# Kernel optimization log

Hardware: AMD Instinct MI355X
Metric: run time of the kernel (lower is better)

## Reference

```python
import jax, jax.numpy as jnp
import numpy as np

# dims: heads, batch, seq (== maxSentenceSize), embed, key/query dim, value dim
H, B, S, E, DK, DV = 16, 4, 1024, 1024, 64, 64
SCALE = int(np.sqrt(DK))  # original uses int(np.sqrt(keySize)) == 8


def setup_inputs() -> dict:
    key = jax.random.key(0)
    k = jax.random.split(key, 5)
    embeddings = jax.random.normal(k[0], (B, S, E), jnp.float32)
    # original init: uniform(0, 1) weights
    Wq = jax.random.uniform(k[1], (H, E, DK), jnp.float32)
    Wk = jax.random.uniform(k[2], (H, E, DK), jnp.float32)
    # note: original valueWeights are also sized (E, keySize)
    Wv = jax.random.uniform(k[3], (H, E, DK), jnp.float32)
    Wo = jax.random.uniform(k[4], (H * DV, E), jnp.float32)
    return {"embeddings": embeddings, "Wq": Wq, "Wk": Wk, "Wv": Wv, "Wo": Wo}


def _causal_mask(s):
    # 0 on/below diagonal, -inf above (matches the torch list-comprehension mask)
    return jnp.where(jnp.tril(jnp.ones((s, s), bool)), 0.0, -jnp.inf).astype(jnp.float32)


def reference(embeddings, Wq, Wk, Wv, Wo):
    # per-head projections, all heads batched: [H,B,S,d]
    q = jnp.einsum('bse,hed->hbsd', embeddings, Wq)
    kk = jnp.einsum('bse,hed->hbsd', embeddings, Wk)
    v = jnp.einsum('bse,hed->hbsd', embeddings, Wv)
    # FAITHFUL to original: keys are RESHAPED (flat reinterpretation [S,DK]->[DK,S]
    # per (head,batch) slice), NOT transposed.
    kT = kk.reshape(H, B, DK, S)
    mask = _causal_mask(S)  # [S,S]
    # softmax((QK_reshaped + mask) / int(sqrt(keySize)))
    scores = (jnp.einsum('hbsd,hbdt->hbst', q, kT) + mask) / SCALE
    attn = jax.nn.softmax(scores, axis=-1)  # [H,B,S,S]
    av = jnp.einsum('hbst,hbtd->hbsd', attn, v)  # [H,B,S,DV]
    # FAITHFUL to original: flat reshape [H,B,S,DV] -> [B,S,DV*H]
    concat = av.reshape(B, S, DV * H)
    return concat @ Wo  # [B,S,E]
```

## Files before the change

kernel.cpp:

```cpp
#include <hip/hip_runtime.h>
#include <math.h>

#define H 16
#define B 4
#define S 1024
#define E 1024
#define DK 64

typedef _Float16 f16x8 __attribute__((ext_vector_type(8)));
typedef _Float16 f16x4 __attribute__((ext_vector_type(4)));
typedef float    f32x4 __attribute__((ext_vector_type(4)));

__device__ __forceinline__ int swzb(int row, int colByte) {
    return row * 128 + (colByte ^ ((row & 7) << 4));
}
__device__ __forceinline__ int swz32(int row, int colByte) {
    int slot = ((row & 3) ^ ((row >> 2) & 3)) << 4;
    return row * 64 + (colByte ^ slot);
}

__device__ __forceinline__ void split8(const float* __restrict__ p,
                                       f16x8& hi, f16x8& lo) {
    float4 a = *(const float4*)p;
    float4 b = *(const float4*)(p + 4);
    float x[8] = {a.x, a.y, a.z, a.w, b.x, b.y, b.z, b.w};
    #pragma unroll
    for (int j = 0; j < 8; ++j) {
        _Float16 h = (_Float16)x[j];
        hi[j] = h;
        lo[j] = (_Float16)(x[j] - (float)h);
    }
}

__global__ __launch_bounds__(256) void cvt_w(const float* __restrict__ Wq,
                                             const float* __restrict__ Wk,
                                             const float* __restrict__ Wv,
                                             _Float16* __restrict__ WTh,
                                             _Float16* __restrict__ WTl) {
    int et = blockIdx.x, chunk = blockIdx.y;
    const float* W = (chunk < 16 ? Wq : chunk < 32 ? Wk : Wv)
                     + (size_t)(chunk & 15) * E * DK;
    __shared__ _Float16 Th[64 * 64];
    __shared__ _Float16 Tl[64 * 64];
    int tid = threadIdx.x;
    #pragma unroll
    for (int rr = 0; rr < 4; ++rr) {
        int u = rr * 256 + tid;
        int ei = u >> 4, f4 = u & 15;
        float4 v = *(const float4*)&W[(size_t)(et * 64 + ei) * 64 + f4 * 4];
        float x[4] = {v.x, v.y, v.z, v.w};
        f16x4 h, l;
        #pragma unroll
        for (int j = 0; j < 4; ++j) {
            _Float16 hh = (_Float16)x[j];
            h[j] = hh;
            l[j] = (_Float16)(x[j] - (float)hh);
        }
        *(f16x4*)((char*)Th + swzb(ei, f4 * 8)) = h;
        *(f16x4*)((char*)Tl + swzb(ei, f4 * 8)) = l;
    }
    __syncthreads();
    #pragma unroll
    for (int rr = 0; rr < 2; ++rr) {
        int u = rr * 256 + tid;
        int d = u >> 3, e8 = u & 7;
        f16x8 oh, ol;
        #pragma unroll
        for (int j = 0; j < 8; ++j) {
            int ei = e8 * 8 + j;
            oh[j] = *(_Float16*)((char*)Th + swzb(ei, d * 2));
            ol[j] = *(_Float16*)((char*)Tl + swzb(ei, d * 2));
        }
        size_t idx = (size_t)(chunk * 64 + d) * 1024 + et * 64 + e8 * 8;
        *(f16x8*)&WTh[idx] = oh;
        if (chunk < 32) *(f16x8*)&WTl[idx] = ol;
    }
}

__global__ __launch_bounds__(256) void cvt_wo(const float* __restrict__ Wo,
                                              _Float16* __restrict__ WoT) {
    int kt = blockIdx.x, nt = blockIdx.y;
    __shared__ _Float16 T[64 * 64];
    int tid = threadIdx.x;
    #pragma unroll
    for (int rr = 0; rr < 4; ++rr) {
        int u = rr * 256 + tid;
        int ki = u >> 4, f4 = u & 15;
        float4 v = *(const float4*)&Wo[(size_t)(kt * 64 + ki) * 1024 + nt * 64 + f4 * 4];
        f16x4 o = { (_Float16)v.x, (_Float16)v.y, (_Float16)v.z, (_Float16)v.w };
        *(f16x4*)((char*)T + swzb(ki, f4 * 8)) = o;
    }
    __syncthreads();
    #pragma unroll
    for (int rr = 0; rr < 2; ++rr) {
        int u = rr * 256 + tid;
        int nl = u >> 3, k8 = u & 7;
        f16x8 o;
        #pragma unroll
        for (int j = 0; j < 8; ++j) {
            int ki = k8 * 8 + j;
            o[j] = *(_Float16*)((char*)T + swzb(ki, nl * 2));
        }
        *(f16x8*)&WoT[(size_t)(nt * 64 + nl) * 1024 + kt * 64 + k8 * 8] = o;
    }
}

__global__ __launch_bounds__(256) void gemm_qkv(
    const float* __restrict__ A, const _Float16* __restrict__ BTh,
    const _Float16* __restrict__ BTl,
    _Float16* __restrict__ QbH, _Float16* __restrict__ QbL,
    _Float16* __restrict__ kkTH, _Float16* __restrict__ kkTL,
    _Float16* __restrict__ V2) {
    __shared__ _Float16 AsH[128 * 32], AsL[128 * 32];
    __shared__ _Float16 BsH[128 * 32], BsL[128 * 32];
    const int NT = 24, cpx = 96;
    int wg = ((int)blockIdx.x & 7) * cpx + ((int)blockIdx.x >> 3);
    int mt = wg / NT, nt = wg % NT;
    const bool qk = (nt < 16);
    int r0 = mt * 128, c0 = nt * 128;
    int tid = threadIdx.x, lane = tid & 63, w = tid >> 6;
    int wr = w >> 1, wc = w & 1;
    int l15 = lane & 15, l4 = lane >> 4;

    f16x8 raH[2], raL[2], rbH[2], rbL[2];
    f32x4 zero = {0.f, 0.f, 0.f, 0.f};
    f32x4 acc[4][4];
    #pragma unroll
    for (int i = 0; i < 4; ++i)
        #pragma unroll
        for (int j = 0; j < 4; ++j) acc[i][j] = zero;

    #pragma unroll
    for (int rr = 0; rr < 2; ++rr) {
        int u = rr * 256 + tid, row = u >> 2, c8 = u & 3;
        split8(&A[(size_t)(r0 + row) * 1024 + c8 * 8], raH[rr], raL[rr]);
        rbH[rr] = *(const f16x8*)&BTh[(size_t)(c0 + row) * 1024 + c8 * 8];
        if (qk) rbL[rr] = *(const f16x8*)&BTl[(size_t)(c0 + row) * 1024 + c8 * 8];
    }

    for (int kt = 0; kt < 32; ++kt) {
        __syncthreads();
        #pragma unroll
        for (int rr = 0; rr < 2; ++rr) {
            int u = rr * 256 + tid, row = u >> 2, cb = (u & 3) * 16;
            int off = swz32(row, cb);
            *(f16x8*)((char*)AsH + off) = raH[rr];
            *(f16x8*)((char*)AsL + off) = raL[rr];
            *(f16x8*)((char*)BsH + off) = rbH[rr];
            if (qk) *(f16x8*)((char*)BsL + off) = rbL[rr];
        }
        if (kt < 31) {
            int k0 = (kt + 1) * 32;
            #pragma unroll
            for (int rr = 0; rr < 2; ++rr) {
                int u = rr * 256 + tid, row = u >> 2, c8 = u & 3;
                split8(&A[(size_t)(r0 + row) * 1024 + k0 + c8 * 8], raH[rr], raL[rr]);
                rbH[rr] = *(const f16x8*)&BTh[(size_t)(c0 + row) * 1024 + k0 + c8 * 8];
                if (qk) rbL[rr] = *(const f16x8*)&BTl[(size_t)(c0 + row) * 1024 + k0 + c8 * 8];
            }
        }
        __syncthreads();
        int kb = l4 * 16;
        f16x8 afH[4], afL[4], bfH[4], bfL[4];
        #pragma unroll
        for (int f = 0; f < 4; ++f) {
            int arow = wr * 64 + f * 16 + l15;
            int brow = wc * 64 + f * 16 + l15;
            afH[f] = *(const f16x8*)((char*)AsH + swz32(arow, kb));
            bfH[f] = *(const f16x8*)((char*)BsH + swz32(brow, kb));
            if (qk) {
                afL[f] = *(const f16x8*)((char*)AsL + swz32(arow, kb));
                bfL[f] = *(const f16x8*)((char*)BsL + swz32(brow, kb));
            }
        }
        #pragma unroll
        for (int i = 0; i < 4; ++i)
            #pragma unroll
            for (int j = 0; j < 4; ++j) {
                acc[i][j] = __builtin_amdgcn_mfma_f32_16x16x32_f16(
                    afH[i], bfH[j], acc[i][j], 0, 0, 0);
                if (qk) {
                    acc[i][j] = __builtin_amdgcn_mfma_f32_16x16x32_f16(
                        afH[i], bfL[j], acc[i][j], 0, 0, 0);
                    acc[i][j] = __builtin_amdgcn_mfma_f32_16x16x32_f16(
                        afL[i], bfH[j], acc[i][j], 0, 0, 0);
                }
            }
    }

    #pragma unroll
    for (int i = 0; i < 4; ++i) {
        int grow0 = r0 + wr * 64 + i * 16 + l4 * 4;
        #pragma unroll
        for (int j = 0; j < 4; ++j) {
            int gcol = c0 + wc * 64 + j * 16 + l15;
            if (gcol < 1024) {
                int hh = gcol >> 6, dk = gcol & 63;
                #pragma unroll
                for (int r = 0; r < 4; ++r) {
                    int grow = grow0 + r;
                    int bb = grow >> 10, s = grow & 1023;
                    float v = acc[i][j][r];
                    _Float16 h = (_Float16)v;
                    size_t idx = (((size_t)hh * 4 + bb) * 1024 + s) * 64 + dk;
                    QbH[idx] = h;
                    QbL[idx] = (_Float16)(v - (float)h);
                }
            } else if (gcol < 2048) {
                int hh = (gcol >> 6) & 15, dk = gcol & 63;
                #pragma unroll
                for (int r = 0; r < 4; ++r) {
                    int grow = grow0 + r;
                    int bb = grow >> 10, s = grow & 1023;
                    float v = acc[i][j][r];
                    _Float16 h = (_Float16)v;
                    size_t idx = (((size_t)hh * 4 + bb) * 64 + (s >> 4)) * 1024
                                 + (s & 15) * 64 + dk;
                    kkTH[idx] = h;
                    kkTL[idx] = (_Float16)(v - (float)h);
                }
            } else {
                int hh = (gcol >> 6) & 15, dv = gcol & 63;
                int bb = grow0 >> 10, s = grow0 & 1023;
                f16x4 o = { (_Float16)acc[i][j][0], (_Float16)acc[i][j][1],
                            (_Float16)acc[i][j][2], (_Float16)acc[i][j][3] };
                *(f16x4*)&V2[(((size_t)hh * 4 + bb) * 64 + dv) * 1024 + s] = o;
            }
        }
    }
}

__global__ __launch_bounds__(256) void trans_k(const _Float16* __restrict__ kkTH,
                                               const _Float16* __restrict__ kkTL,
                                               _Float16* __restrict__ K2H,
                                               _Float16* __restrict__ K2L) {
    int tt = blockIdx.x;
    size_t hb = blockIdx.y;
    int mode = blockIdx.z;
    const _Float16* src = mode ? kkTL : kkTH;
    _Float16* dst = mode ? K2L : K2H;
    __shared__ _Float16 T[64 * 64];
    int tid = threadIdx.x;
    #pragma unroll
    for (int rr = 0; rr < 2; ++rr) {
        int u = rr * 256 + tid;
        int d = u >> 3, c8 = u & 7;
        f16x8 v = *(const f16x8*)&src[(hb * 64 + d) * 1024 + tt * 64 + c8 * 8];
        *(f16x8*)((char*)T + swzb(d, c8 * 16)) = v;
    }
    __syncthreads();
    #pragma unroll
    for (int rr = 0; rr < 2; ++rr) {
        int u = rr * 256 + tid;
        int ti = u >> 3, d8 = u & 7;
        f16x8 o;
        #pragma unroll
        for (int j = 0; j < 8; ++j)
            o[j] = *(_Float16*)((char*)T + swzb(d8 * 8 + j, ti * 2));
        *(f16x8*)&dst[(hb * 1024 + tt * 64 + ti) * 64 + d8 * 8] = o;
    }
}

__global__ __launch_bounds__(256) void attn(
    const _Float16* __restrict__ QbH, const _Float16* __restrict__ QbL,
    const _Float16* __restrict__ K2H, const _Float16* __restrict__ K2L,
    const _Float16* __restrict__ V2, _Float16* __restrict__ CC) {
    int qt = blockIdx.x, b = blockIdx.y, h = blockIdx.z;
    size_t hb = (size_t)h * 4 + b;
    __shared__ _Float16 QsH[64 * 64], QsL[64 * 64];
    __shared__ _Float16 KsH[64 * 64], KsL[64 * 64];
    __shared__ _Float16 Vs[64 * 64], Ps[64 * 64];
    int tid = threadIdx.x, lane = tid & 63, w = tid >> 6;
    int l15 = lane & 15, l4 = lane >> 4;
    int s0 = qt * 64;

    #pragma unroll
    for (int rr = 0; rr < 2; ++rr) {
        int u = rr * 256 + tid, row = u >> 3, c8 = u & 7;
        size_t gi = (hb * 1024 + s0 + row) * 64 + c8 * 8;
        int off = swzb(row, c8 * 16);
        *(f16x8*)((char*)QsH + off) = *(const f16x8*)&QbH[gi];
        *(f16x8*)((char*)QsL + off) = *(const f16x8*)&QbL[gi];
    }
    __syncthreads();
    int srow = w * 16 + l15;
    f16x8 qfH[2], qfL[2];
    #pragma unroll
    for (int ks = 0; ks < 2; ++ks) {
        int kb = (ks * 32 + l4 * 8) * 2;
        qfH[ks] = *(const f16x8*)((char*)QsH + swzb(srow, kb));
        qfL[ks] = *(const f16x8*)((char*)QsL + swzb(srow, kb));
    }

    float m = -__builtin_inff(), lsum = 0.f;
    f32x4 zero = {0.f, 0.f, 0.f, 0.f};
    f32x4 acc2[4] = {zero, zero, zero, zero};
    int sg = s0 + srow;
    int ntile = qt + 1;

    for (int tt = 0; tt < ntile; ++tt) {
        int t0 = tt * 64;
        __syncthreads();
        #pragma unroll
        for (int rr = 0; rr < 2; ++rr) {
            int u = rr * 256 + tid, row = u >> 3, c8 = u & 7;
            int off = swzb(row, c8 * 16);
            size_t ki = (hb * 1024 + t0 + row) * 64 + c8 * 8;
            *(f16x8*)((char*)KsH + off) = *(const f16x8*)&K2H[ki];
            *(f16x8*)((char*)KsL + off) = *(const f16x8*)&K2L[ki];
            *(f16x8*)((char*)Vs + off) =
                *(const f16x8*)&V2[(hb * 64 + row) * 1024 + t0 + c8 * 8];
        }
        __syncthreads();

        f32x4 z[4] = {zero, zero, zero, zero};
        #pragma unroll
        for (int ks = 0; ks < 2; ++ks) {
            int kb = (ks * 32 + l4 * 8) * 2;
            #pragma unroll
            for (int f = 0; f < 4; ++f) {
                int trow = f * 16 + l15;
                f16x8 akH = *(const f16x8*)((char*)KsH + swzb(trow, kb));
                f16x8 akL = *(const f16x8*)((char*)KsL + swzb(trow, kb));
                z[f] = __builtin_amdgcn_mfma_f32_16x16x32_f16(akH, qfH[ks], z[f], 0, 0, 0);
                z[f] = __builtin_amdgcn_mfma_f32_16x16x32_f16(akH, qfL[ks], z[f], 0, 0, 0);
                z[f] = __builtin_amdgcn_mfma_f32_16x16x32_f16(akL, qfH[ks], z[f], 0, 0, 0);
            }
        }
        float mt = -__builtin_inff();
        #pragma unroll
        for (int f = 0; f < 4; ++f)
            #pragma unroll
            for (int r = 0; r < 4; ++r) {
                int tg = t0 + f * 16 + l4 * 4 + r;
                float val = z[f][r] * 0.125f;
                val = (tg > sg) ? -__builtin_inff() : val;
                z[f][r] = val;
                mt = fmaxf(mt, val);
            }
        mt = fmaxf(mt, __shfl_xor(mt, 16));
        mt = fmaxf(mt, __shfl_xor(mt, 32));
        float mn = fmaxf(m, mt);
        float corr = __expf(m - mn);
        float ps = 0.f;
        #pragma unroll
        for (int f = 0; f < 4; ++f)
            #pragma unroll
            for (int r = 0; r < 4; ++r) {
                float p = __expf(z[f][r] - mn);
                z[f][r] = p;
                ps += p;
            }
        ps += __shfl_xor(ps, 16);
        ps += __shfl_xor(ps, 32);
        lsum = lsum * corr + ps;
        m = mn;
        #pragma unroll
        for (int f = 0; f < 4; ++f) acc2[f] *= corr;

        #pragma unroll
        for (int f = 0; f < 4; ++f) {
            f16x4 pk = { (_Float16)z[f][0], (_Float16)z[f][1],
                         (_Float16)z[f][2], (_Float16)z[f][3] };
            *(f16x4*)((char*)Ps + swzb(srow, (f * 16 + l4 * 4) * 2)) = pk;
        }
        #pragma unroll
        for (int ks = 0; ks < 2; ++ks) {
            int kb = (ks * 32 + l4 * 8) * 2;
            f16x8 bp = *(const f16x8*)((char*)Ps + swzb(srow, kb));
            #pragma unroll
            for (int f = 0; f < 4; ++f) {
                int dvrow = f * 16 + l15;
                f16x8 av = *(const f16x8*)((char*)Vs + swzb(dvrow, kb));
                acc2[f] = __builtin_amdgcn_mfma_f32_16x16x32_f16(av, bp, acc2[f], 0, 0, 0);
            }
        }
    }

    float inv = 1.f / lsum;
    int sp = s0 + srow;
    int bprow = h >> 2;
    int spp = (h & 3) * 256 + b * 64 + (sp >> 4);
    int cb = (sp & 15) * 64;
    #pragma unroll
    for (int f = 0; f < 4; ++f) {
        int dv = f * 16 + l4 * 4;
        f16x4 o = { (_Float16)(acc2[f][0] * inv), (_Float16)(acc2[f][1] * inv),
                    (_Float16)(acc2[f][2] * inv), (_Float16)(acc2[f][3] * inv) };
        *(f16x4*)&CC[((size_t)bprow * 1024 + spp) * 1024 + cb + dv] = o;
    }
}

__global__ __launch_bounds__(256) void gemm_out(
    const _Float16* __restrict__ A, const _Float16* __restrict__ BT,
    float* __restrict__ out) {
    __shared__ _Float16 As[128 * 64];
    __shared__ _Float16 Bs[128 * 64];
    const int NT = 8, cpx = 32;
    int wg = ((int)blockIdx.x & 7) * cpx + ((int)blockIdx.x >> 3);
    int mt = wg / NT, nt = wg % NT;
    int r0 = mt * 128, c0 = nt * 128;
    int tid = threadIdx.x, lane = tid & 63, w = tid >> 6;
    int wr = w >> 1, wc = w & 1;
    int l15 = lane & 15, l4 = lane >> 4;

    f16x8 ra[4], rb[4];
    f32x4 zero = {0.f, 0.f, 0.f, 0.f};
    f32x4 acc[4][4];
    #pragma unroll
    for (int i = 0; i < 4; ++i)
        #pragma unroll
        for (int j = 0; j < 4; ++j) acc[i][j] = zero;

    #pragma unroll
    for (int rr = 0; rr < 4; ++rr) {
        int u = rr * 256 + tid, row = u >> 3, c8 = u & 7;
        ra[rr] = *(const f16x8*)&A [(size_t)(r0 + row) * 1024 + c8 * 8];
        rb[rr] = *(const f16x8*)&BT[(size_t)(c0 + row) * 1024 + c8 * 8];
    }

    for (int kt = 0; kt < 16; ++kt) {
        __syncthreads();
        #pragma unroll
        for (int rr = 0; rr < 4; ++rr) {
            int u = rr * 256 + tid, row = u >> 3, c8 = u & 7;
            int off = swzb(row, c8 * 16);
            *(f16x8*)((char*)As + off) = ra[rr];
            *(f16x8*)((char*)Bs + off) = rb[rr];
        }
        if (kt < 15) {
            int k0 = (kt + 1) * 64;
            #pragma unroll
            for (int rr = 0; rr < 4; ++rr) {
                int u = rr * 256 + tid, row = u >> 3, c8 = u & 7;
                ra[rr] = *(const f16x8*)&A [(size_t)(r0 + row) * 1024 + k0 + c8 * 8];
                rb[rr] = *(const f16x8*)&BT[(size_t)(c0 + row) * 1024 + k0 + c8 * 8];
            }
        }
        __syncthreads();
        #pragma unroll
        for (int ks = 0; ks < 2; ++ks) {
            int kb = (ks * 32 + l4 * 8) * 2;
            f16x8 af[4], bf[4];
            #pragma unroll
            for (int f = 0; f < 4; ++f) {
                int arow = wr * 64 + f * 16 + l15;
                int brow = wc * 64 + f * 16 + l15;
                af[f] = *(const f16x8*)((char*)As + swzb(arow, kb));
                bf[f] = *(const f16x8*)((char*)Bs + swzb(brow, kb));
            }
            #pragma unroll
            for (int i = 0; i < 4; ++i)
                #pragma unroll
                for (int j = 0; j < 4; ++j)
                    acc[i][j] = __builtin_amdgcn_mfma_f32_16x16x32_f16(
                        af[i], bf[j], acc[i][j], 0, 0, 0);
        }
    }

    #pragma unroll
    for (int i = 0; i < 4; ++i) {
        int grow0 = r0 + wr * 64 + i * 16 + l4 * 4;
        #pragma unroll
        for (int j = 0; j < 4; ++j) {
            int gcol = c0 + wc * 64 + j * 16 + l15;
            #pragma unroll
            for (int r = 0; r < 4; ++r)
                out[(size_t)(grow0 + r) * 1024 + gcol] = acc[i][j][r];
        }
    }
}

extern "C" void kernel_launch(void* const* d_in, const int* in_sizes, int n_in,
                              void* d_out, int out_size, void* d_ws, size_t ws_size,
                              hipStream_t stream) {
    const float* emb = (const float*)d_in[0];
    const float* Wq  = (const float*)d_in[1];
    const float* Wk  = (const float*)d_in[2];
    const float* Wv  = (const float*)d_in[3];
    const float* Wo  = (const float*)d_in[4];
    float* out = (float*)d_out;

    _Float16* WTh = (_Float16*)d_ws;
    _Float16* WTl = WTh + 3145728;
    _Float16* WoT = WTl + 2097152;
    _Float16* QbH = WoT + 1048576;
    _Float16* QbL = QbH + 4194304;
    _Float16* K2H = QbL + 4194304;
    _Float16* K2L = K2H + 4194304;
    _Float16* V2  = K2L + 4194304;
    _Float16* CC  = V2  + 4194304;
    _Float16* kkTH = (_Float16*)d_out;
    _Float16* kkTL = kkTH + 4194304;

    cvt_w   <<<dim3(16, 48), 256, 0, stream>>>(Wq, Wk, Wv, WTh, WTl);
    cvt_wo  <<<dim3(16, 16), 256, 0, stream>>>(Wo, WoT);
    gemm_qkv<<<768, 256, 0, stream>>>(emb, WTh, WTl, QbH, QbL, kkTH, kkTL, V2);
    trans_k <<<dim3(16, 64, 2), 256, 0, stream>>>(kkTH, kkTL, K2H, K2L);
    attn    <<<dim3(16, 4, 16), 256, 0, stream>>>(QbH, QbL, K2H, K2L, V2, CC);
    gemm_out<<<256, 256, 0, stream>>>(CC, WoT, out);
}
```

Before: 262.0 us.

## Pre-split embeddings, split QKV GEMM, use direct global-to-LDS loads, prefetch attention tiles

The embedding fp16 hi/lo split moves into a separate pre-pass, and the two weight-conversion kernels are merged into one launch. The fused QKV GEMM is split into a three-MFMA Q/K GEMM and a single-precision V GEMM with smaller tiles, so the V path no longer branches. The GEMMs now load tiles with global_load_lds straight into unswizzled LDS instead of staging through registers, which removes register prefetch but may add bank conflicts and loses the load/compute overlap. The attention kernel register-prefetches the next K/V tile, reverses query-tile order so long causal tiles start first, and raises wave priority around the MFMA blocks. Workspace buffers are also aliased to cut memory use.

```diff
diff --git a/kernel.cpp b/kernel.cpp
--- a/kernel.cpp
+++ b/kernel.cpp
@@ -14,115 +14,109 @@
 __device__ __forceinline__ int swzb(int row, int colByte) {
     return row * 128 + (colByte ^ ((row & 7) << 4));
 }
-__device__ __forceinline__ int swz32(int row, int colByte) {
-    int slot = ((row & 3) ^ ((row >> 2) & 3)) << 4;
-    return row * 64 + (colByte ^ slot);
-}
-
-__device__ __forceinline__ void split8(const float* __restrict__ p,
-                                       f16x8& hi, f16x8& lo) {
-    float4 a = *(const float4*)p;
-    float4 b = *(const float4*)(p + 4);
+
+__global__ __launch_bounds__(256) void cvt_split_emb(const float* __restrict__ in,
+                                                     _Float16* __restrict__ outH,
+                                                     _Float16* __restrict__ outL) {
+    int i = (blockIdx.x * 256 + threadIdx.x) * 8;
+    float4 a = *(const float4*)&in[i];
+    float4 b = *(const float4*)&in[i + 4];
     float x[8] = {a.x, a.y, a.z, a.w, b.x, b.y, b.z, b.w};
+    f16x8 h, l;
     #pragma unroll
     for (int j = 0; j < 8; ++j) {
-        _Float16 h = (_Float16)x[j];
-        hi[j] = h;
-        lo[j] = (_Float16)(x[j] - (float)h);
-    }
-}
-
-__global__ __launch_bounds__(256) void cvt_w(const float* __restrict__ Wq,
-                                             const float* __restrict__ Wk,
-                                             const float* __restrict__ Wv,
-                                             _Float16* __restrict__ WTh,
-                                             _Float16* __restrict__ WTl) {
-    int et = blockIdx.x, chunk = blockIdx.y;
-    const float* W = (chunk < 16 ? Wq : chunk < 32 ? Wk : Wv)
-                     + (size_t)(chunk & 15) * E * DK;
+        _Float16 hh = (_Float16)x[j];
+        h[j] = hh;
+        l[j] = (_Float16)(x[j] - (float)hh);
+    }
+    *(f16x8*)&outH[i] = h;
+    *(f16x8*)&outL[i] = l;
+}
+
+__global__ __launch_bounds__(256) void cvt_weights(
+    const float* __restrict__ Wq, const float* __restrict__ Wk,
+    const float* __restrict__ Wv, const float* __restrict__ Wo,
+    _Float16* __restrict__ WTh, _Float16* __restrict__ WTl,
+    _Float16* __restrict__ WoT) {
     __shared__ _Float16 Th[64 * 64];
     __shared__ _Float16 Tl[64 * 64];
     int tid = threadIdx.x;
-    #pragma unroll
-    for (int rr = 0; rr < 4; ++rr) {
-        int u = rr * 256 + tid;
-        int ei = u >> 4, f4 = u & 15;
-        float4 v = *(const float4*)&W[(size_t)(et * 64 + ei) * 64 + f4 * 4];
-        float x[4] = {v.x, v.y, v.z, v.w};
-        f16x4 h, l;
-        #pragma unroll
-        for (int j = 0; j < 4; ++j) {
-            _Float16 hh = (_Float16)x[j];
-            h[j] = hh;
-            l[j] = (_Float16)(x[j] - (float)hh);
-        }
-        *(f16x4*)((char*)Th + swzb(ei, f4 * 8)) = h;
-        *(f16x4*)((char*)Tl + swzb(ei, f4 * 8)) = l;
-    }
-    __syncthreads();
-    #pragma unroll
-    for (int rr = 0; rr < 2; ++rr) {
-        int u = rr * 256 + tid;
-        int d = u >> 3, e8 = u & 7;
-        f16x8 oh, ol;
-        #pragma unroll
-        for (int j = 0; j < 8; ++j) {
-            int ei = e8 * 8 + j;
-            oh[j] = *(_Float16*)((char*)Th + swzb(ei, d * 2));
-            ol[j] = *(_Float16*)((char*)Tl + swzb(ei, d * 2));
-        }
-        size_t idx = (size_t)(chunk * 64 + d) * 1024 + et * 64 + e8 * 8;
-        *(f16x8*)&WTh[idx] = oh;
-        if (chunk < 32) *(f16x8*)&WTl[idx] = ol;
-    }
-}
-
-__global__ __launch_bounds__(256) void cvt_wo(const float* __restrict__ Wo,
-                                              _Float16* __restrict__ WoT) {
-    int kt = blockIdx.x, nt = blockIdx.y;
-    __shared__ _Float16 T[64 * 64];
-    int tid = threadIdx.x;
-    #pragma unroll
-    for (int rr = 0; rr < 4; ++rr) {
-        int u = rr * 256 + tid;
-        int ki = u >> 4, f4 = u & 15;
-        float4 v = *(const float4*)&Wo[(size_t)(kt * 64 + ki) * 1024 + nt * 64 + f4 * 4];
-        f16x4 o = { (_Float16)v.x, (_Float16)v.y, (_Float16)v.z, (_Float16)v.w };
-        *(f16x4*)((char*)T + swzb(ki, f4 * 8)) = o;
-    }
-    __syncthreads();
-    #pragma unroll
-    for (int rr = 0; rr < 2; ++rr) {
-        int u = rr * 256 + tid;
-        int nl = u >> 3, k8 = u & 7;
-        f16x8 o;
-        #pragma unroll
-        for (int j = 0; j < 8; ++j) {
-            int ki = k8 * 8 + j;
-            o[j] = *(_Float16*)((char*)T + swzb(ki, nl * 2));
-        }
-        *(f16x8*)&WoT[(size_t)(nt * 64 + nl) * 1024 + kt * 64 + k8 * 8] = o;
-    }
-}
-
-__global__ __launch_bounds__(256) void gemm_qkv(
-    const float* __restrict__ A, const _Float16* __restrict__ BTh,
-    const _Float16* __restrict__ BTl,
+    if (blockIdx.y < 48) {
+        int et = blockIdx.x, chunk = blockIdx.y;
+        const float* W = (chunk < 16 ? Wq : chunk < 32 ? Wk : Wv)
+                         + (size_t)(chunk & 15) * E * DK;
+        #pragma unroll
+        for (int rr = 0; rr < 4; ++rr) {
+            int u = rr * 256 + tid;
+            int ei = u >> 4, f4 = u & 15;
+            float4 v = *(const float4*)&W[(size_t)(et * 64 + ei) * 64 + f4 * 4];
+            float x[4] = {v.x, v.y, v.z, v.w};
+            f16x4 h, l;
+            #pragma unroll
+            for (int j = 0; j < 4; ++j) {
+                _Float16 hh = (_Float16)x[j];
+                h[j] = hh;
+                l[j] = (_Float16)(x[j] - (float)hh);
+            }
+            *(f16x4*)((char*)Th + swzb(ei, f4 * 8)) = h;
+            *(f16x4*)((char*)Tl + swzb(ei, f4 * 8)) = l;
+        }
+        __syncthreads();
+        #pragma unroll
+        for (int rr = 0; rr < 2; ++rr) {
+            int u = rr * 256 + tid;
+            int d = u >> 3, e8 = u & 7;
+            f16x8 oh, ol;
+            #pragma unroll
+            for (int j = 0; j < 8; ++j) {
+                int ei = e8 * 8 + j;
+                oh[j] = *(_Float16*)((char*)Th + swzb(ei, d * 2));
+                ol[j] = *(_Float16*)((char*)Tl + swzb(ei, d * 2));
+            }
+            size_t idx = (size_t)(chunk * 64 + d) * 1024 + et * 64 + e8 * 8;
+            *(f16x8*)&WTh[idx] = oh;
+            if (chunk < 32) *(f16x8*)&WTl[idx] = ol;
+        }
+    } else {
+        int kt = blockIdx.x, nt = blockIdx.y - 48;
+        #pragma unroll
+        for (int rr = 0; rr < 4; ++rr) {
+            int u = rr * 256 + tid;
+            int ki = u >> 4, f4 = u & 15;
+            float4 v = *(const float4*)&Wo[(size_t)(kt * 64 + ki) * 1024 + nt * 64 + f4 * 4];
+            f16x4 o = { (_Float16)v.x, (_Float16)v.y, (_Float16)v.z, (_Float16)v.w };
+            *(f16x4*)((char*)Th + swzb(ki, f4 * 8)) = o;
+        }
+        __syncthreads();
+        #pragma unroll
+        for (int rr = 0; rr < 2; ++rr) {
+            int u = rr * 256 + tid;
+            int nl = u >> 3, k8 = u & 7;
+            f16x8 o;
+            #pragma unroll
+            for (int j = 0; j < 8; ++j) {
+                int ki = k8 * 8 + j;
+                o[j] = *(_Float16*)((char*)Th + swzb(ki, nl * 2));
+            }
+            *(f16x8*)&WoT[(size_t)(nt * 64 + nl) * 1024 + kt * 64 + k8 * 8] = o;
+        }
+    }
+}
+
+__global__ __launch_bounds__(256) void gemm_qk(
+    const _Float16* __restrict__ AH, const _Float16* __restrict__ AL,
+    const _Float16* __restrict__ BTh, const _Float16* __restrict__ BTl,
     _Float16* __restrict__ QbH, _Float16* __restrict__ QbL,
-    _Float16* __restrict__ kkTH, _Float16* __restrict__ kkTL,
-    _Float16* __restrict__ V2) {
+    _Float16* __restrict__ kkTH, _Float16* __restrict__ kkTL) {
     __shared__ _Float16 AsH[128 * 32], AsL[128 * 32];
     __shared__ _Float16 BsH[128 * 32], BsL[128 * 32];
-    const int NT = 24, cpx = 96;
-    int wg = ((int)blockIdx.x & 7) * cpx + ((int)blockIdx.x >> 3);
-    int mt = wg / NT, nt = wg % NT;
-    const bool qk = (nt < 16);
+    int wg = ((int)blockIdx.x & 7) * 64 + ((int)blockIdx.x >> 3);
+    int mt = wg >> 4, nt = wg & 15;
     int r0 = mt * 128, c0 = nt * 128;
     int tid = threadIdx.x, lane = tid & 63, w = tid >> 6;
     int wr = w >> 1, wc = w & 1;
     int l15 = lane & 15, l4 = lane >> 4;
 
-    f16x8 raH[2], raL[2], rbH[2], rbL[2];
     f32x4 zero = {0.f, 0.f, 0.f, 0.f};
     f32x4 acc[4][4];
     #pragma unroll
@@ -130,48 +124,31 @@
         #pragma unroll
         for (int j = 0; j < 4; ++j) acc[i][j] = zero;
 
-    #pragma unroll
-    for (int rr = 0; rr < 2; ++rr) {
-        int u = rr * 256 + tid, row = u >> 2, c8 = u & 3;
-        split8(&A[(size_t)(r0 + row) * 1024 + c8 * 8], raH[rr], raL[rr]);
-        rbH[rr] = *(const f16x8*)&BTh[(size_t)(c0 + row) * 1024 + c8 * 8];
-        if (qk) rbL[rr] = *(const f16x8*)&BTl[(size_t)(c0 + row) * 1024 + c8 * 8];
-    }
-
     for (int kt = 0; kt < 32; ++kt) {
         __syncthreads();
         #pragma unroll
         for (int rr = 0; rr < 2; ++rr) {
-            int u = rr * 256 + tid, row = u >> 2, cb = (u & 3) * 16;
-            int off = swz32(row, cb);
-            *(f16x8*)((char*)AsH + off) = raH[rr];
-            *(f16x8*)((char*)AsL + off) = raL[rr];
-            *(f16x8*)((char*)BsH + off) = rbH[rr];
-            if (qk) *(f16x8*)((char*)BsL + off) = rbL[rr];
-        }
-        if (kt < 31) {
-            int k0 = (kt + 1) * 32;
-            #pragma unroll
-            for (int rr = 0; rr < 2; ++rr) {
-                int u = rr * 256 + tid, row = u >> 2, c8 = u & 3;
-                split8(&A[(size_t)(r0 + row) * 1024 + k0 + c8 * 8], raH[rr], raL[rr]);
-                rbH[rr] = *(const f16x8*)&BTh[(size_t)(c0 + row) * 1024 + k0 + c8 * 8];
-                if (qk) rbL[rr] = *(const f16x8*)&BTl[(size_t)(c0 + row) * 1024 + k0 + c8 * 8];
-            }
-        }
-        __syncthreads();
+            int u = rr * 256 + tid;
+            int row = u >> 2, c8 = u & 3;
+            size_t ga = (size_t)(r0 + row) * 1024 + kt * 32 + c8 * 8;
+            size_t gb = (size_t)(c0 + row) * 1024 + kt * 32 + c8 * 8;
+            __builtin_amdgcn_global_load_lds(&AH[ga],  &AsH[u * 8], 16, 0, 0);
+            __builtin_amdgcn_global_load_lds(&AL[ga],  &AsL[u * 8], 16, 0, 0);
+            __builtin_amdgcn_global_load_lds(&BTh[gb], &BsH[u * 8], 16, 0, 0);
+            __builtin_amdgcn_global_load_lds(&BTl[gb], &BsL[u * 8], 16, 0, 0);
+        }
+        __syncthreads();
+
         int kb = l4 * 16;
         f16x8 afH[4], afL[4], bfH[4], bfL[4];
         #pragma unroll
         for (int f = 0; f < 4; ++f) {
-            int arow = wr * 64 + f * 16 + l15;
-            int brow = wc * 64 + f * 16 + l15;
-            afH[f] = *(const f16x8*)((char*)AsH + swz32(arow, kb));
-            bfH[f] = *(const f16x8*)((char*)BsH + swz32(brow, kb));
-            if (qk) {
-                afL[f] = *(const f16x8*)((char*)AsL + swz32(arow, kb));
-                bfL[f] = *(const f16x8*)((char*)BsL + swz32(brow, kb));
-            }
+            int ar = wr * 64 + f * 16 + l15;
+            int br = wc * 64 + f * 16 + l15;
+            afH[f] = *(const f16x8*)((char*)AsH + ar * 64 + kb);
+            afL[f] = *(const f16x8*)((char*)AsL + ar * 64 + kb);
+            bfH[f] = *(const f16x8*)((char*)BsH + br * 64 + kb);
+            bfL[f] = *(const f16x8*)((char*)BsL + br * 64 + kb);
         }
         #pragma unroll
         for (int i = 0; i < 4; ++i)
@@ -179,12 +156,10 @@
             for (int j = 0; j < 4; ++j) {
                 acc[i][j] = __builtin_amdgcn_mfma_f32_16x16x32_f16(
                     afH[i], bfH[j], acc[i][j], 0, 0, 0);
-                if (qk) {
-                    acc[i][j] = __builtin_amdgcn_mfma_f32_16x16x32_f16(
-                        afH[i], bfL[j], acc[i][j], 0, 0, 0);
-                    acc[i][j] = __builtin_amdgcn_mfma_f32_16x16x32_f16(
-                        afL[i], bfH[j], acc[i][j], 0, 0, 0);
-                }
+                acc[i][j] = __builtin_amdgcn_mfma_f32_16x16x32_f16(
+                    afH[i], bfL[j], acc[i][j], 0, 0, 0);
+                acc[i][j] = __builtin_amdgcn_mfma_f32_16x16x32_f16(
+                    afL[i], bfH[j], acc[i][j], 0, 0, 0);
             }
     }
 
@@ -206,7 +181,7 @@
                     QbH[idx] = h;
                     QbL[idx] = (_Float16)(v - (float)h);
                 }
-            } else if (gcol < 2048) {
+            } else {
                 int hh = (gcol >> 6) & 15, dk = gcol & 63;
                 #pragma unroll
                 for (int r = 0; r < 4; ++r) {
@@ -219,13 +194,78 @@
                     kkTH[idx] = h;
                     kkTL[idx] = (_Float16)(v - (float)h);
                 }
-            } else {
-                int hh = (gcol >> 6) & 15, dv = gcol & 63;
-                int bb = grow0 >> 10, s = grow0 & 1023;
-                f16x4 o = { (_Float16)acc[i][j][0], (_Float16)acc[i][j][1],
-                            (_Float16)acc[i][j][2], (_Float16)acc[i][j][3] };
-                *(f16x4*)&V2[(((size_t)hh * 4 + bb) * 64 + dv) * 1024 + s] = o;
-            }
+            }
+        }
+    }
+}
+
+__global__ __launch_bounds__(256) void gemm_v(
+    const _Float16* __restrict__ AH, const _Float16* __restrict__ BTh,
+    _Float16* __restrict__ V2) {
+    __shared__ _Float16 As[128 * 32];
+    __shared__ _Float16 Bs[64 * 32];
+    int wg = ((int)blockIdx.x & 7) * 64 + ((int)blockIdx.x >> 3);
+    int mt = wg >> 4, nt = wg & 15;
+    int r0 = mt * 128, c0 = nt * 64;
+    int tid = threadIdx.x, lane = tid & 63, w = tid >> 6;
+    int wr = w >> 1, wc = w & 1;
+    int l15 = lane & 15, l4 = lane >> 4;
+
+    f32x4 zero = {0.f, 0.f, 0.f, 0.f};
+    f32x4 acc[4][2];
+    #pragma unroll
+    for (int i = 0; i < 4; ++i)
+        #pragma unroll
+        for (int j = 0; j < 2; ++j) acc[i][j] = zero;
+
+    for (int kt = 0; kt < 32; ++kt) {
+        __syncthreads();
+        #pragma unroll
+        for (int rr = 0; rr < 2; ++rr) {
+            int u = rr * 256 + tid;
+            int row = u >> 2, c8 = u & 3;
+            size_t ga = (size_t)(r0 + row) * 1024 + kt * 32 + c8 * 8;
+            __builtin_amdgcn_global_load_lds(&AH[ga], &As[u * 8], 16, 0, 0);
+        }
+        {
+            int u = tid;
+            int row = u >> 2, c8 = u & 3;
+            size_t gb = (size_t)(2048 + c0 + row) * 1024 + kt * 32 + c8 * 8;
+            __builtin_amdgcn_global_load_lds(&BTh[gb], &Bs[u * 8], 16, 0, 0);
+        }
+        __syncthreads();
+
+        int kb = l4 * 16;
+        f16x8 af[4], bf[2];
+        #pragma unroll
+        for (int f = 0; f < 4; ++f) {
+            int ar = wr * 64 + f * 16 + l15;
+            af[f] = *(const f16x8*)((char*)As + ar * 64 + kb);
+        }
+        #pragma unroll
+        for (int j = 0; j < 2; ++j) {
+            int br = wc * 32 + j * 16 + l15;
+            bf[j] = *(const f16x8*)((char*)Bs + br * 64 + kb);
+        }
+        #pragma unroll
+        for (int i = 0; i < 4; ++i)
+            #pragma unroll
+            for (int j = 0; j < 2; ++j)
+                acc[i][j] = __builtin_amdgcn_mfma_f32_16x16x32_f16(
+                    af[i], bf[j], acc[i][j], 0, 0, 0);
+    }
+
+    #pragma unroll
+    for (int i = 0; i < 4; ++i) {
+        int grow0 = r0 + wr * 64 + i * 16 + l4 * 4;
+        int bb = grow0 >> 10, s = grow0 & 1023;
+        #pragma unroll
+        for (int j = 0; j < 2; ++j) {
+            int gcol = c0 + wc * 32 + j * 16 + l15;
+            int hh = gcol >> 6, dv = gcol & 63;
+            f16x4 o = { (_Float16)acc[i][j][0], (_Float16)acc[i][j][1],
+                        (_Float16)acc[i][j][2], (_Float16)acc[i][j][3] };
+            *(f16x4*)&V2[(((size_t)hh * 4 + bb) * 64 + dv) * 1024 + s] = o;
         }
     }
 }
@@ -265,7 +305,8 @@
     const _Float16* __restrict__ QbH, const _Float16* __restrict__ QbL,
     const _Float16* __restrict__ K2H, const _Float16* __restrict__ K2L,
     const _Float16* __restrict__ V2, _Float16* __restrict__ CC) {
-    int qt = blockIdx.x, b = blockIdx.y, h = blockIdx.z;
+    int qt = 15 - (int)blockIdx.x;
+    int b = blockIdx.y, h = blockIdx.z;
     size_t hb = (size_t)h * 4 + b;
     __shared__ _Float16 QsH[64 * 64], QsL[64 * 64];
     __shared__ _Float16 KsH[64 * 64], KsL[64 * 64];
@@ -282,6 +323,15 @@
         *(f16x8*)((char*)QsH + off) = *(const f16x8*)&QbH[gi];
         *(f16x8*)((char*)QsL + off) = *(const f16x8*)&QbL[gi];
     }
+    f16x8 rkH[2], rkL[2], rv[2];
+    #pragma unroll
+    for (int rr = 0; rr < 2; ++rr) {
+        int u = rr * 256 + tid, row = u >> 3, c8 = u & 7;
+        size_t ki = (hb * 1024 + row) * 64 + c8 * 8;
+        rkH[rr] = *(const f16x8*)&K2H[ki];
+        rkL[rr] = *(const f16x8*)&K2L[ki];
+        rv[rr]  = *(const f16x8*)&V2[(hb * 64 + row) * 1024 + c8 * 8];
+    }
     __syncthreads();
     int srow = w * 16 + l15;
     f16x8 qfH[2], qfL[2];
@@ -305,15 +355,25 @@
         for (int rr = 0; rr < 2; ++rr) {
             int u = rr * 256 + tid, row = u >> 3, c8 = u & 7;
             int off = swzb(row, c8 * 16);
-            size_t ki = (hb * 1024 + t0 + row) * 64 + c8 * 8;
-            *(f16x8*)((char*)KsH + off) = *(const f16x8*)&K2H[ki];
-            *(f16x8*)((char*)KsL + off) = *(const f16x8*)&K2L[ki];
-            *(f16x8*)((char*)Vs + off) =
-                *(const f16x8*)&V2[(hb * 64 + row) * 1024 + t0 + c8 * 8];
+            *(f16x8*)((char*)KsH + off) = rkH[rr];
+            *(f16x8*)((char*)KsL + off) = rkL[rr];
+            *(f16x8*)((char*)Vs + off)  = rv[rr];
+        }
+        if (tt + 1 < ntile) {
+            int t0n = t0 + 64;
+            #pragma unroll
+            for (int rr = 0; rr < 2; ++rr) {
+                int u = rr * 256 + tid, row = u >> 3, c8 = u & 7;
+                size_t ki = (hb * 1024 + t0n + row) * 64 + c8 * 8;
+                rkH[rr] = *(const f16x8*)&K2H[ki];
+                rkL[rr] = *(const f16x8*)&K2L[ki];
+                rv[rr]  = *(const f16x8*)&V2[(hb * 64 + row) * 1024 + t0n + c8 * 8];
+            }
         }
         __syncthreads();
 
         f32x4 z[4] = {zero, zero, zero, zero};
+        __builtin_amdgcn_s_setprio(1);
         #pragma unroll
         for (int ks = 0; ks < 2; ++ks) {
             int kb = (ks * 32 + l4 * 8) * 2;
@@ -327,6 +387,7 @@
                 z[f] = __builtin_amdgcn_mfma_f32_16x16x32_f16(akL, qfH[ks], z[f], 0, 0, 0);
             }
         }
+        __builtin_amdgcn_s_setprio(0);
         float mt = -__builtin_inff();
         #pragma unroll
         for (int f = 0; f < 4; ++f)
@@ -364,6 +425,7 @@
                          (_Float16)z[f][2], (_Float16)z[f][3] };
             *(f16x4*)((char*)Ps + swzb(srow, (f * 16 + l4 * 4) * 2)) = pk;
         }
+        __builtin_amdgcn_s_setprio(1);
         #pragma unroll
         for (int ks = 0; ks < 2; ++ks) {
             int kb = (ks * 32 + l4 * 8) * 2;
@@ -375,6 +437,7 @@
                 acc2[f] = __builtin_amdgcn_mfma_f32_16x16x32_f16(av, bp, acc2[f], 0, 0, 0);
             }
         }
+        __builtin_amdgcn_s_setprio(0);
     }
 
     float inv = 1.f / lsum;
@@ -396,15 +459,13 @@
     float* __restrict__ out) {
     __shared__ _Float16 As[128 * 64];
     __shared__ _Float16 Bs[128 * 64];
-    const int NT = 8, cpx = 32;
-    int wg = ((int)blockIdx.x & 7) * cpx + ((int)blockIdx.x >> 3);
-    int mt = wg / NT, nt = wg % NT;
+    int wg = ((int)blockIdx.x & 7) * 32 + ((int)blockIdx.x >> 3);
+    int mt = wg >> 3, nt = wg & 7;
     int r0 = mt * 128, c0 = nt * 128;
     int tid = threadIdx.x, lane = tid & 63, w = tid >> 6;
     int wr = w >> 1, wc = w & 1;
     int l15 = lane & 15, l4 = lane >> 4;
 
-    f16x8 ra[4], rb[4];
     f32x4 zero = {0.f, 0.f, 0.f, 0.f};
     f32x4 acc[4][4];
     #pragma unroll
@@ -412,42 +473,29 @@
         #pragma unroll
         for (int j = 0; j < 4; ++j) acc[i][j] = zero;
 
-    #pragma unroll
-    for (int rr = 0; rr < 4; ++rr) {
-        int u = rr * 256 + tid, row = u >> 3, c8 = u & 7;
-        ra[rr] = *(const f16x8*)&A [(size_t)(r0 + row) * 1024 + c8 * 8];
-        rb[rr] = *(const f16x8*)&BT[(size_t)(c0 + row) * 1024 + c8 * 8];
-    }
-
     for (int kt = 0; kt < 16; ++kt) {
         __syncthreads();
         #pragma unroll
         for (int rr = 0; rr < 4; ++rr) {
-            int u = rr * 256 + tid, row = u >> 3, c8 = u & 7;
-            int off = swzb(row, c8 * 16);
-            *(f16x8*)((char*)As + off) = ra[rr];
-            *(f16x8*)((char*)Bs + off) = rb[rr];
-        }
-        if (kt < 15) {
-            int k0 = (kt + 1) * 64;
-            #pragma unroll
-            for (int rr = 0; rr < 4; ++rr) {
-                int u = rr * 256 + tid, row = u >> 3, c8 = u & 7;
-                ra[rr] = *(const f16x8*)&A [(size_t)(r0 + row) * 1024 + k0 + c8 * 8];
-                rb[rr] = *(const f16x8*)&BT[(size_t)(c0 + row) * 1024 + k0 + c8 * 8];
-            }
-        }
-        __syncthreads();
+            int u = rr * 256 + tid;
+            int row = u >> 3, c8 = u & 7;
+            size_t ga = (size_t)(r0 + row) * 1024 + kt * 64 + c8 * 8;
+            size_t gb = (size_t)(c0 + row) * 1024 + kt * 64 + c8 * 8;
+            __builtin_amdgcn_global_load_lds(&A[ga],  &As[u * 8], 16, 0, 0);
+            __builtin_amdgcn_global_load_lds(&BT[gb], &Bs[u * 8], 16, 0, 0);
+        }
+        __syncthreads();
+
         #pragma unroll
         for (int ks = 0; ks < 2; ++ks) {
             int kb = (ks * 32 + l4 * 8) * 2;
             f16x8 af[4], bf[4];
             #pragma unroll
             for (int f = 0; f < 4; ++f) {
-                int arow = wr * 64 + f * 16 + l15;
-                int brow = wc * 64 + f * 16 + l15;
-                af[f] = *(const f16x8*)((char*)As + swzb(arow, kb));
-                bf[f] = *(const f16x8*)((char*)Bs + swzb(brow, kb));
+                int ar = wr * 64 + f * 16 + l15;
+                int br = wc * 64 + f * 16 + l15;
+                af[f] = *(const f16x8*)((char*)As + ar * 128 + kb);
+                bf[f] = *(const f16x8*)((char*)Bs + br * 128 + kb);
             }
             #pragma unroll
             for (int i = 0; i < 4; ++i)
@@ -481,22 +529,25 @@
     const float* Wo  = (const float*)d_in[4];
     float* out = (float*)d_out;
 
-    _Float16* WTh = (_Float16*)d_ws;
-    _Float16* WTl = WTh + 3145728;
-    _Float16* WoT = WTl + 2097152;
-    _Float16* QbH = WoT + 1048576;
-    _Float16* QbL = QbH + 4194304;
-    _Float16* K2H = QbL + 4194304;
-    _Float16* K2L = K2H + 4194304;
-    _Float16* V2  = K2L + 4194304;
-    _Float16* CC  = V2  + 4194304;
+    _Float16* embH = (_Float16*)d_ws;
+    _Float16* embL = embH + 4194304;
+    _Float16* WTh  = embL + 4194304;
+    _Float16* WTl  = WTh + 3145728;
+    _Float16* WoT  = WTl + 2097152;
+    _Float16* QbH  = WoT + 1048576;
+    _Float16* QbL  = QbH + 4194304;
+    _Float16* V2   = QbL + 4194304;
+    _Float16* K2H  = embH;
+    _Float16* K2L  = embL;
+    _Float16* CC   = WTh;
     _Float16* kkTH = (_Float16*)d_out;
     _Float16* kkTL = kkTH + 4194304;
 
-    cvt_w   <<<dim3(16, 48), 256, 0, stream>>>(Wq, Wk, Wv, WTh, WTl);
-    cvt_wo  <<<dim3(16, 16), 256, 0, stream>>>(Wo, WoT);
-    gemm_qkv<<<768, 256, 0, stream>>>(emb, WTh, WTl, QbH, QbL, kkTH, kkTL, V2);
-    trans_k <<<dim3(16, 64, 2), 256, 0, stream>>>(kkTH, kkTL, K2H, K2L);
-    attn    <<<dim3(16, 4, 16), 256, 0, stream>>>(QbH, QbL, K2H, K2L, V2, CC);
-    gemm_out<<<256, 256, 0, stream>>>(CC, WoT, out);
-}
+    cvt_split_emb<<<2048, 256, 0, stream>>>(emb, embH, embL);
+    cvt_weights  <<<dim3(16, 64), 256, 0, stream>>>(Wq, Wk, Wv, Wo, WTh, WTl, WoT);
+    gemm_qk      <<<512, 256, 0, stream>>>(embH, embL, WTh, WTl, QbH, QbL, kkTH, kkTL);
+    gemm_v       <<<512, 256, 0, stream>>>(embH, WTh, V2);
+    trans_k      <<<dim3(16, 64, 2), 256, 0, stream>>>(kkTH, kkTL, K2H, K2L);
+    attn         <<<dim3(16, 4, 16), 256, 0, stream>>>(QbH, QbL, K2H, K2L, V2, CC);
+    gemm_out     <<<256, 256, 0, stream>>>(CC, WoT, out);
+}
```

Result: faster. 253.3 us (-3.3%).
